# Optimization experiments

Measured on AMD Instinct MI355X. Metric: run time of the kernel, lower is better.

Reference implementation:

```python
import jax, jax.numpy as jnp
import numpy as np

N_NODES = 50000
N_EDGES = 800000
BASIS = 64
HIDDEN_RO = 128
N_GRAPHS = 512
T = 3


def setup_inputs() -> dict:
    key = jax.random.key(0)
    ks = jax.random.split(key, 12)
    Z = jax.random.randint(ks[0], (N_NODES,), 0, 10)
    edge_index = jax.random.randint(ks[1], (2, N_EDGES), 0, N_NODES)
    edge_attr = jax.random.normal(ks[2], (N_EDGES, BASIS), dtype=jnp.float32)
    batch = jnp.sort(jax.random.randint(ks[3], (N_NODES,), 0, N_GRAPHS))
    s = 1.0 / np.sqrt(BASIS)
    embed = jax.random.normal(ks[4], (10, BASIS), dtype=jnp.float32)
    cfW = jax.random.uniform(ks[5], (BASIS, BASIS), jnp.float32, -s, s)
    cfb = jax.random.uniform(ks[6], (BASIS,), jnp.float32, -s, s)
    dfW = jax.random.uniform(ks[7], (BASIS, BASIS), jnp.float32, -s, s)
    dfb = jax.random.uniform(ks[8], (BASIS,), jnp.float32, -s, s)
    fcW = jax.random.uniform(ks[9], (BASIS, BASIS), jnp.float32, -s, s)  # no bias
    W1 = jax.random.uniform(ks[10], (BASIS, HIDDEN_RO), jnp.float32, -s, s)
    b1 = jnp.zeros((HIDDEN_RO,), jnp.float32)
    W2 = jax.random.uniform(ks[11], (HIDDEN_RO, 4), jnp.float32, -1.0 / np.sqrt(HIDDEN_RO), 1.0 / np.sqrt(HIDDEN_RO))
    b2 = jnp.zeros((4,), jnp.float32)
    return {"Z": Z, "edge_index": edge_index, "edge_attr": edge_attr, "batch": batch,
            "embed": embed, "cfW": cfW, "cfb": cfb, "dfW": dfW, "dfb": dfb, "fcW": fcW,
            "W1": W1, "b1": b1, "W2": W2, "b2": b2}


def reference(Z, edge_index, edge_attr, batch, embed, cfW, cfb, dfW, dfb, fcW, W1, b1, W2, b2):
    src, dst = edge_index[0], edge_index[1]  # x_j gathered from src, aggregated at dst
    C = embed[Z]  # [N, basis]
    # df(edge_attr) does not depend on C; compute once (same math, shared weights)
    d_feat = edge_attr @ dfW + dfb  # [E, basis]
    for _ in range(T):
        c_feat = C[src] @ cfW + cfb            # gather + linear  [E, basis]
        msg = jnp.tanh((c_feat * d_feat) @ fcW)  # [E, basis]
        agg = jax.ops.segment_sum(msg, dst, num_segments=N_NODES)
        C = C + agg
    h = jnp.tanh(C @ W1 + b1) @ W2 + b2        # readout MLP [N, 4]
    return jax.ops.segment_sum(h, batch, num_segments=N_GRAPHS)  # global_add_pool [G, 4]
```

## Files before the change

kernel.cpp:

```cpp
#include <hip/hip_runtime.h>
#include <math.h>

#define N_NODES   50000
#define N_EDGES   800000
#define BASIS     64
#define HIDDEN_RO 128
#define N_GRAPHS  512
#define T_ITERS   3

typedef short s8 __attribute__((ext_vector_type(8)));
typedef float f4 __attribute__((ext_vector_type(4)));

#define MFMA16(a, b, c) __builtin_amdgcn_mfma_f32_16x16x32_bf16(a, b, c, 0, 0, 0)

__device__ __forceinline__ float fast_tanh(float x) {
    float e = __expf(2.0f * x);
    return 1.0f - 2.0f / (e + 1.0f);
}

__device__ __forceinline__ f4 splat4(float x) { f4 v; v[0]=x; v[1]=x; v[2]=x; v[3]=x; return v; }

__device__ __forceinline__ void split8(const float* x, s8& hi, s8& lo) {
    union { unsigned a[4]; s8 v; } H, L;
    #pragma unroll
    for (int j = 0; j < 4; ++j) {
        float e0 = x[2*j], e1 = x[2*j+1];
        unsigned u0 = __float_as_uint(e0), u1 = __float_as_uint(e1);
        H.a[j] = (u0 >> 16) | (u1 & 0xFFFF0000u);
        float l0 = e0 - __uint_as_float(u0 & 0xFFFF0000u);
        float l1 = e1 - __uint_as_float(u1 & 0xFFFF0000u);
        L.a[j] = (__float_as_uint(l0) >> 16) | (__float_as_uint(l1) & 0xFFFF0000u);
    }
    hi = H.v; lo = L.v;
}

__device__ __forceinline__ void load_wfrags(const float* __restrict__ W, int lane,
                                            s8 whi[2][4], s8 wlo[2][4]) {
    int q = lane >> 4, c = lane & 15;
    #pragma unroll
    for (int ks = 0; ks < 2; ++ks)
        #pragma unroll
        for (int g = 0; g < 4; ++g) {
            float t[8];
            #pragma unroll
            for (int j = 0; j < 8; ++j)
                t[j] = W[(ks*32 + q*8 + j) * 64 + g*16 + c];
            split8(t, whi[ks][g], wlo[ks][g]);
        }
}

__global__ void k_init_C(const int* __restrict__ Z, const float* __restrict__ embed,
                         float* __restrict__ C) {
    int i = blockIdx.x * blockDim.x + threadIdx.x;
    if (i >= N_NODES * BASIS) return;
    int n = i >> 6, c = i & 63;
    C[i] = embed[Z[n] * BASIS + c];
}

__global__ __launch_bounds__(256) void k_gemm64(const float* __restrict__ in,
        const float* __restrict__ W, const float* __restrict__ b,
        float* __restrict__ out, int rows) {
    int lane = threadIdx.x & 63, wv = threadIdx.x >> 6;
    int q = lane >> 4, c = lane & 15;
    s8 whi[2][4], wlo[2][4];
    load_wfrags(W, lane, whi, wlo);
    float bias[4];
    #pragma unroll
    for (int g = 0; g < 4; ++g) bias[g] = b[g*16 + c];
    int chunks = (rows + 15) >> 4;
    int wave = blockIdx.x * 4 + wv, nw = gridDim.x * 4;
    for (int ch = wave; ch < chunks; ch += nw) {
        int base = ch << 4;
        int row = base + c;
        bool valid = row < rows;
        const float4* ip = (const float4*)(in + (size_t)(valid ? row : 0) * 64);
        s8 ahi[2], alo[2];
        #pragma unroll
        for (int ks = 0; ks < 2; ++ks) {
            float4 a0 = ip[ks*8 + q*2 + 0];
            float4 a1 = ip[ks*8 + q*2 + 1];
            float xs[8] = {a0.x,a0.y,a0.z,a0.w, a1.x,a1.y,a1.z,a1.w};
            if (!valid) {
                #pragma unroll
                for (int j = 0; j < 8; ++j) xs[j] = 0.0f;
            }
            split8(xs, ahi[ks], alo[ks]);
        }
        f4 acc[4];
        #pragma unroll
        for (int g = 0; g < 4; ++g) acc[g] = splat4(bias[g]);
        #pragma unroll
        for (int ks = 0; ks < 2; ++ks)
            #pragma unroll
            for (int g = 0; g < 4; ++g) {
                acc[g] = MFMA16(ahi[ks], whi[ks][g], acc[g]);
                acc[g] = MFMA16(ahi[ks], wlo[ks][g], acc[g]);
                acc[g] = MFMA16(alo[ks], whi[ks][g], acc[g]);
            }
        #pragma unroll
        for (int g = 0; g < 4; ++g)
            #pragma unroll
            for (int r = 0; r < 4; ++r) {
                int ro = base + q*4 + r;
                if (ro < rows) out[(size_t)ro * 64 + g*16 + c] = acc[g][r];
            }
    }
}

__global__ void k_hist(const int* __restrict__ dst, int* __restrict__ deg) {
    int e = blockIdx.x * blockDim.x + threadIdx.x;
    if (e < N_EDGES) atomicAdd(&deg[dst[e]], 1);
}

__global__ void k_scan(const int* __restrict__ deg, int* __restrict__ off,
                       int* __restrict__ cursor) {
    __shared__ int wsum[16];
    __shared__ int run_s;
    int t = threadIdx.x, lane = t & 63, w = t >> 6;
    if (t == 0) run_s = 0;
    __syncthreads();
    for (int base = 0; base < N_NODES; base += 1024) {
        int i = base + t;
        int v = (i < N_NODES) ? deg[i] : 0;
        int s = v;
        #pragma unroll
        for (int ofs = 1; ofs < 64; ofs <<= 1) {
            int tmp = __shfl_up(s, ofs, 64);
            if (lane >= ofs) s += tmp;
        }
        if (lane == 63) wsum[w] = s;
        __syncthreads();
        if (w == 0) {
            int x = (lane < 16) ? wsum[lane] : 0;
            #pragma unroll
            for (int ofs = 1; ofs < 16; ofs <<= 1) {
                int tmp = __shfl_up(x, ofs, 64);
                if (lane >= ofs) x += tmp;
            }
            if (lane < 16) wsum[lane] = x;
        }
        __syncthreads();
        int run = run_s;
        int wex = (w == 0) ? 0 : wsum[w - 1];
        int incl = run + wex + s;
        if (i < N_NODES) { off[i] = incl - v; cursor[i] = incl - v; }
        __syncthreads();
        if (t == 1023) run_s = incl;
        __syncthreads();
    }
    if (t == 0) off[N_NODES] = run_s;
}

__global__ void k_fill(const int* __restrict__ dst, int* __restrict__ cursor,
                       int* __restrict__ eid) {
    int e = blockIdx.x * blockDim.x + threadIdx.x;
    if (e < N_EDGES) {
        int p = atomicAdd(&cursor[dst[e]], 1);
        eid[p] = e;
    }
}

__global__ __launch_bounds__(256) void k_mp_mfma(const float* __restrict__ CF,
        const float* __restrict__ DF, const float* __restrict__ fcW,
        const int* __restrict__ src, const int* __restrict__ off,
        const int* __restrict__ eid, float* __restrict__ C) {
    int lane = threadIdx.x & 63, wv = threadIdx.x >> 6;
    int q = lane >> 4, c = lane & 15;
    s8 whi[2][4], wlo[2][4];
    load_wfrags(fcW, lane, whi, wlo);
    int wave = blockIdx.x * 4 + wv, nw = gridDim.x * 4;
    for (int n = wave; n < N_NODES; n += nw) {
        int beg = off[n], end = off[n + 1];
        float acc0 = 0.f, acc1 = 0.f, acc2 = 0.f, acc3 = 0.f;
        #pragma unroll 1
        for (int base = beg; base < end; base += 16) {
            int cnt = end - base;
            bool valid = c < cnt;
            int idx = base + (valid ? c : 0);
            int e = eid[idx];
            int s = src[e];
            const float4* cfp = (const float4*)(CF + (size_t)s * 64);
            const float4* dfp = (const float4*)(DF + (size_t)e * 64);
            s8 ahi[2], alo[2];
            #pragma unroll
            for (int ks = 0; ks < 2; ++ks) {
                float4 c0 = cfp[ks*8 + q*2 + 0];
                float4 c1 = cfp[ks*8 + q*2 + 1];
                float4 d0 = dfp[ks*8 + q*2 + 0];
                float4 d1 = dfp[ks*8 + q*2 + 1];
                float xs[8] = {c0.x*d0.x, c0.y*d0.y, c0.z*d0.z, c0.w*d0.w,
                               c1.x*d1.x, c1.y*d1.y, c1.z*d1.z, c1.w*d1.w};
                if (!valid) {
                    #pragma unroll
                    for (int j = 0; j < 8; ++j) xs[j] = 0.0f;
                }
                split8(xs, ahi[ks], alo[ks]);
            }
            f4 d[4];
            #pragma unroll
            for (int g = 0; g < 4; ++g) d[g] = splat4(0.0f);
            #pragma unroll
            for (int ks = 0; ks < 2; ++ks)
                #pragma unroll
                for (int g = 0; g < 4; ++g) {
                    d[g] = MFMA16(ahi[ks], whi[ks][g], d[g]);
                    d[g] = MFMA16(ahi[ks], wlo[ks][g], d[g]);
                    d[g] = MFMA16(alo[ks], whi[ks][g], d[g]);
                }
            acc0 += fast_tanh(d[0][0]) + fast_tanh(d[0][1]) + fast_tanh(d[0][2]) + fast_tanh(d[0][3]);
            acc1 += fast_tanh(d[1][0]) + fast_tanh(d[1][1]) + fast_tanh(d[1][2]) + fast_tanh(d[1][3]);
            acc2 += fast_tanh(d[2][0]) + fast_tanh(d[2][1]) + fast_tanh(d[2][2]) + fast_tanh(d[2][3]);
            acc3 += fast_tanh(d[3][0]) + fast_tanh(d[3][1]) + fast_tanh(d[3][2]) + fast_tanh(d[3][3]);
        }
        acc0 += __shfl_xor(acc0, 16, 64); acc0 += __shfl_xor(acc0, 32, 64);
        acc1 += __shfl_xor(acc1, 16, 64); acc1 += __shfl_xor(acc1, 32, 64);
        acc2 += __shfl_xor(acc2, 16, 64); acc2 += __shfl_xor(acc2, 32, 64);
        acc3 += __shfl_xor(acc3, 16, 64); acc3 += __shfl_xor(acc3, 32, 64);
        float v = (q == 0) ? acc0 : (q == 1) ? acc1 : (q == 2) ? acc2 : acc3;
        C[(size_t)n * 64 + lane] += v;
    }
}

__global__ __launch_bounds__(256) void k_edge_fb(const float* __restrict__ CF,
        const float* __restrict__ ea, const float* __restrict__ dfW,
        const float* __restrict__ dfb, const float* __restrict__ fcW,
        const int* __restrict__ src, const int* __restrict__ dst,
        float* __restrict__ C) {
    int e = blockIdx.x * blockDim.x + threadIdx.x;
    if (e >= N_EDGES) return;
    int s = src[e], d = dst[e];
    float dfeat[BASIS];
    #pragma unroll
    for (int c = 0; c < BASIS; ++c) dfeat[c] = dfb[c];
    const float4* ea4 = (const float4*)(ea + (size_t)e * BASIS);
    #pragma unroll
    for (int k0 = 0; k0 < 16; ++k0) {
        float4 xv = ea4[k0];
        #pragma unroll
        for (int c = 0; c < BASIS; ++c)
            dfeat[c] += xv.x * dfW[(4*k0+0)*64+c] + xv.y * dfW[(4*k0+1)*64+c]
                      + xv.z * dfW[(4*k0+2)*64+c] + xv.w * dfW[(4*k0+3)*64+c];
    }
    const float4* cf4 = (const float4*)(CF + (size_t)s * BASIS);
    float acc[BASIS];
    #pragma unroll
    for (int c = 0; c < BASIS; ++c) acc[c] = 0.0f;
    #pragma unroll
    for (int k0 = 0; k0 < 16; ++k0) {
        float4 a = cf4[k0];
        float x0 = a.x * dfeat[4*k0+0], x1 = a.y * dfeat[4*k0+1];
        float x2 = a.z * dfeat[4*k0+2], x3 = a.w * dfeat[4*k0+3];
        #pragma unroll
        for (int c = 0; c < BASIS; ++c)
            acc[c] += x0 * fcW[(4*k0+0)*64+c] + x1 * fcW[(4*k0+1)*64+c]
                    + x2 * fcW[(4*k0+2)*64+c] + x3 * fcW[(4*k0+3)*64+c];
    }
    float* crow = C + (size_t)d * BASIS;
    #pragma unroll
    for (int c = 0; c < BASIS; ++c) atomicAdd(&crow[c], fast_tanh(acc[c]));
}

__global__ __launch_bounds__(256) void k_readout2(const float* __restrict__ C,
        const float* __restrict__ W1, const float* __restrict__ b1,
        const float* __restrict__ W2, const float* __restrict__ b2,
        const int* __restrict__ batch, float* __restrict__ out) {
    __shared__ float w1[BASIS * HIDDEN_RO];
    __shared__ float xbuf[4][64];
    int t = threadIdx.x;
    for (int i = t; i < BASIS * HIDDEN_RO; i += 256) w1[i] = W1[i];
    __syncthreads();
    int lane = t & 63, wv = t >> 6;
    float b1a = b1[lane], b1b = b1[64 + lane];
    float4 w2a = ((const float4*)W2)[lane];
    float4 w2b = ((const float4*)W2)[64 + lane];
    int wave = blockIdx.x * 4 + wv;
    int nw   = gridDim.x * 4;
    for (int n = wave; n < N_NODES; n += nw) {
        float x = C[(size_t)n * 64 + lane];
        xbuf[wv][lane] = x;
        __builtin_amdgcn_wave_barrier();
        const float4* xb = (const float4*)xbuf[wv];
        float sa = b1a, sb = b1b;
        #pragma unroll
        for (int k4 = 0; k4 < 16; ++k4) {
            float4 xv = xb[k4];
            const float* r0 = &w1[(4*k4 + 0) * HIDDEN_RO];
            const float* r1 = &w1[(4*k4 + 1) * HIDDEN_RO];
            const float* r2 = &w1[(4*k4 + 2) * HIDDEN_RO];
            const float* r3 = &w1[(4*k4 + 3) * HIDDEN_RO];
            sa += xv.x * r0[lane]      + xv.y * r1[lane]
                + xv.z * r2[lane]      + xv.w * r3[lane];
            sb += xv.x * r0[64 + lane] + xv.y * r1[64 + lane]
                + xv.z * r2[64 + lane] + xv.w * r3[64 + lane];
        }
        float ha = fast_tanh(sa), hb = fast_tanh(sb);
        float v0 = ha * w2a.x + hb * w2b.x;
        float v1 = ha * w2a.y + hb * w2b.y;
        float v2 = ha * w2a.z + hb * w2b.z;
        float v3 = ha * w2a.w + hb * w2b.w;
        #pragma unroll
        for (int ofs = 32; ofs >= 1; ofs >>= 1) {
            v0 += __shfl_down(v0, ofs, 64);
            v1 += __shfl_down(v1, ofs, 64);
            v2 += __shfl_down(v2, ofs, 64);
            v3 += __shfl_down(v3, ofs, 64);
        }
        if (lane == 0) {
            int g = batch[n];
            atomicAdd(&out[(size_t)g * 4 + 0], v0);
            atomicAdd(&out[(size_t)g * 4 + 1], v1);
            atomicAdd(&out[(size_t)g * 4 + 2], v2);
            atomicAdd(&out[(size_t)g * 4 + 3], v3);
        }
        __builtin_amdgcn_wave_barrier();
    }
}

extern "C" void kernel_launch(void* const* d_in, const int* in_sizes, int n_in,
                              void* d_out, int out_size, void* d_ws, size_t ws_size,
                              hipStream_t stream) {
    const int*   Z     = (const int*)d_in[0];
    const int*   ei    = (const int*)d_in[1];
    const float* ea    = (const float*)d_in[2];
    const int*   batch = (const int*)d_in[3];
    const float* embed = (const float*)d_in[4];
    const float* cfW   = (const float*)d_in[5];
    const float* cfb   = (const float*)d_in[6];
    const float* dfW   = (const float*)d_in[7];
    const float* dfb   = (const float*)d_in[8];
    const float* fcW   = (const float*)d_in[9];
    const float* W1    = (const float*)d_in[10];
    const float* b1    = (const float*)d_in[11];
    const float* W2    = (const float*)d_in[12];
    const float* b2    = (const float*)d_in[13];
    const int* src = ei;
    const int* dst = ei + N_EDGES;
    float* out = (float*)d_out;

    const size_t bC = (size_t)N_NODES * BASIS * sizeof(float);
    const size_t bE = (size_t)N_EDGES * sizeof(int);
    const size_t bO = (size_t)(N_NODES + 1) * sizeof(int);
    char* p = (char*)d_ws;
    float* C      = (float*)p;  p += bC;
    float* CF     = (float*)p;  p += bC;
    int*   eid    = (int*)p;    p += bE;
    int*   deg    = (int*)p;    p += bO;
    int*   off    = (int*)p;    p += bO;
    int*   cursor = (int*)p;    p += bO;
    float* DF     = (float*)p;
    const size_t need = (size_t)(p - (char*)d_ws) + (size_t)N_EDGES * BASIS * sizeof(float);
    const bool full = ws_size >= need;

    hipMemsetAsync(d_out, 0, (size_t)out_size * sizeof(float), stream);
    k_init_C<<<(N_NODES * BASIS + 255) / 256, 256, 0, stream>>>(Z, embed, C);

    if (full) {
        hipMemsetAsync(deg, 0, bO, stream);
        k_hist<<<(N_EDGES + 255) / 256, 256, 0, stream>>>(dst, deg);
        k_scan<<<1, 1024, 0, stream>>>(deg, off, cursor);
        k_fill<<<(N_EDGES + 255) / 256, 256, 0, stream>>>(dst, cursor, eid);
        k_gemm64<<<4096, 256, 0, stream>>>(ea, dfW, dfb, DF, N_EDGES);
        for (int t = 0; t < T_ITERS; ++t) {
            k_gemm64<<<800, 256, 0, stream>>>(C, cfW, cfb, CF, N_NODES);
            k_mp_mfma<<<2048, 256, 0, stream>>>(CF, DF, fcW, src, off, eid, C);
        }
    } else {
        for (int t = 0; t < T_ITERS; ++t) {
            k_gemm64<<<800, 256, 0, stream>>>(C, cfW, cfb, CF, N_NODES);
            k_edge_fb<<<(N_EDGES + 255) / 256, 256, 0, stream>>>(CF, ea, dfW, dfb, fcW, src, dst, C);
        }
    }

    k_readout2<<<512, 256, 0, stream>>>(C, W1, b1, W2, b2, batch, out);
}
```

Baseline: 979.4 us.

## Store DF in CSR order and process multi-node edge windows with LDS accumulation

The edge-feature GEMM now writes DF permuted into dst-sorted CSR order, using a packed int4 meta array (edge, src, dst). The message-passing kernel then reads DF contiguously instead of through an eid indirection. Each wave handles 4 consecutive nodes as one dense stream of 16-edge windows, which avoids padding waste on low-degree nodes. Results go into shared-memory accumulators through LDS atomics, and the next window's loads are software-prefetched. The costs are extra meta bandwidth, a gathered read of edge_attr, and LDS atomic contention.

```diff
diff --git a/kernel.cpp b/kernel.cpp
--- a/kernel.cpp
+++ b/kernel.cpp
@@ -7,6 +7,8 @@
 #define HIDDEN_RO 128
 #define N_GRAPHS  512
 #define T_ITERS   3
+#define R_NODES   4
+#define MP_BLOCKS (N_NODES / R_NODES / 4)
 
 typedef short s8 __attribute__((ext_vector_type(8)));
 typedef float f4 __attribute__((ext_vector_type(4)));
@@ -104,6 +106,49 @@
                 int ro = base + q*4 + r;
                 if (ro < rows) out[(size_t)ro * 64 + g*16 + c] = acc[g][r];
             }
+    }
+}
+
+__global__ __launch_bounds__(256) void k_gemm64g(const float* __restrict__ in,
+        const int4* __restrict__ meta, const float* __restrict__ W,
+        const float* __restrict__ b, float* __restrict__ out) {
+    int lane = threadIdx.x & 63, wv = threadIdx.x >> 6;
+    int q = lane >> 4, c = lane & 15;
+    s8 whi[2][4], wlo[2][4];
+    load_wfrags(W, lane, whi, wlo);
+    float bias[4];
+    #pragma unroll
+    for (int g = 0; g < 4; ++g) bias[g] = b[g*16 + c];
+    const int windows = N_EDGES / 16;
+    int wave = blockIdx.x * 4 + wv, nw = gridDim.x * 4;
+    for (int wb = wave; wb < windows; wb += nw) {
+        int slot = wb * 16 + c;
+        int e = meta[slot].x;
+        const float4* ip = (const float4*)(in + (size_t)e * 64);
+        s8 ahi[2], alo[2];
+        #pragma unroll
+        for (int ks = 0; ks < 2; ++ks) {
+            float4 a0 = ip[ks*8 + q*2 + 0];
+            float4 a1 = ip[ks*8 + q*2 + 1];
+            float xs[8] = {a0.x,a0.y,a0.z,a0.w, a1.x,a1.y,a1.z,a1.w};
+            split8(xs, ahi[ks], alo[ks]);
+        }
+        f4 acc[4];
+        #pragma unroll
+        for (int g = 0; g < 4; ++g) acc[g] = splat4(bias[g]);
+        #pragma unroll
+        for (int ks = 0; ks < 2; ++ks)
+            #pragma unroll
+            for (int g = 0; g < 4; ++g) {
+                acc[g] = MFMA16(ahi[ks], whi[ks][g], acc[g]);
+                acc[g] = MFMA16(ahi[ks], wlo[ks][g], acc[g]);
+                acc[g] = MFMA16(alo[ks], whi[ks][g], acc[g]);
+            }
+        #pragma unroll
+        for (int g = 0; g < 4; ++g)
+            #pragma unroll
+            for (int r = 0; r < 4; ++r)
+                out[(size_t)(wb*16 + q*4 + r) * 64 + g*16 + c] = acc[g][r];
     }
 }
 
@@ -151,73 +196,109 @@
     if (t == 0) off[N_NODES] = run_s;
 }
 
-__global__ void k_fill(const int* __restrict__ dst, int* __restrict__ cursor,
-                       int* __restrict__ eid) {
+__global__ void k_fill(const int* __restrict__ src, const int* __restrict__ dst,
+                       int* __restrict__ cursor, int4* __restrict__ meta) {
     int e = blockIdx.x * blockDim.x + threadIdx.x;
     if (e < N_EDGES) {
-        int p = atomicAdd(&cursor[dst[e]], 1);
-        eid[p] = e;
-    }
-}
-
-__global__ __launch_bounds__(256) void k_mp_mfma(const float* __restrict__ CF,
+        int d = dst[e], s = src[e];
+        int p = atomicAdd(&cursor[d], 1);
+        meta[p] = make_int4(e, s, d, 0);
+    }
+}
+
+__global__ __launch_bounds__(256) void k_mp_win(const float* __restrict__ CF,
         const float* __restrict__ DF, const float* __restrict__ fcW,
-        const int* __restrict__ src, const int* __restrict__ off,
-        const int* __restrict__ eid, float* __restrict__ C) {
+        const int4* __restrict__ meta, const int* __restrict__ off,
+        float* __restrict__ C) {
+    __shared__ float acc[4][R_NODES + 1][64];
     int lane = threadIdx.x & 63, wv = threadIdx.x >> 6;
     int q = lane >> 4, c = lane & 15;
     s8 whi[2][4], wlo[2][4];
     load_wfrags(fcW, lane, whi, wlo);
-    int wave = blockIdx.x * 4 + wv, nw = gridDim.x * 4;
-    for (int n = wave; n < N_NODES; n += nw) {
-        int beg = off[n], end = off[n + 1];
-        float acc0 = 0.f, acc1 = 0.f, acc2 = 0.f, acc3 = 0.f;
-        #pragma unroll 1
-        for (int base = beg; base < end; base += 16) {
-            int cnt = end - base;
-            bool valid = c < cnt;
-            int idx = base + (valid ? c : 0);
-            int e = eid[idx];
-            int s = src[e];
-            const float4* cfp = (const float4*)(CF + (size_t)s * 64);
-            const float4* dfp = (const float4*)(DF + (size_t)e * 64);
-            s8 ahi[2], alo[2];
-            #pragma unroll
-            for (int ks = 0; ks < 2; ++ks) {
-                float4 c0 = cfp[ks*8 + q*2 + 0];
-                float4 c1 = cfp[ks*8 + q*2 + 1];
-                float4 d0 = dfp[ks*8 + q*2 + 0];
-                float4 d1 = dfp[ks*8 + q*2 + 1];
-                float xs[8] = {c0.x*d0.x, c0.y*d0.y, c0.z*d0.z, c0.w*d0.w,
-                               c1.x*d1.x, c1.y*d1.y, c1.z*d1.z, c1.w*d1.w};
-                if (!valid) {
-                    #pragma unroll
-                    for (int j = 0; j < 8; ++j) xs[j] = 0.0f;
-                }
-                split8(xs, ahi[ks], alo[ks]);
-            }
-            f4 d[4];
-            #pragma unroll
-            for (int g = 0; g < 4; ++g) d[g] = splat4(0.0f);
-            #pragma unroll
-            for (int ks = 0; ks < 2; ++ks)
+    int wave = blockIdx.x * 4 + wv;
+    int n0 = wave * R_NODES;
+    int sbeg = off[n0], send = off[n0 + R_NODES];
+    #pragma unroll
+    for (int r = 0; r <= R_NODES; ++r) acc[wv][r][lane] = 0.0f;
+    __builtin_amdgcn_wave_barrier();
+    int nwin = (send - sbeg + 15) >> 4;
+
+    int4 m0 = make_int4(0,0,0,0), m1 = m0;
+    float4 dc[4], cf[4];
+    if (nwin > 0) {
+        int sl0 = sbeg + c; if (sl0 >= send) sl0 = send - 1;
+        m0 = meta[sl0];
+        if (nwin > 1) {
+            int sl1 = sbeg + 16 + c; if (sl1 >= send) sl1 = send - 1;
+            m1 = meta[sl1];
+        }
+        const float4* dp = (const float4*)(DF + (size_t)sl0 * 64);
+        dc[0] = dp[q*2]; dc[1] = dp[q*2+1]; dc[2] = dp[8+q*2]; dc[3] = dp[8+q*2+1];
+        const float4* cp = (const float4*)(CF + (size_t)m0.y * 64);
+        cf[0] = cp[q*2]; cf[1] = cp[q*2+1]; cf[2] = cp[8+q*2]; cf[3] = cp[8+q*2+1];
+    }
+    #pragma unroll 1
+    for (int w = 0; w < nwin; ++w) {
+        int base = sbeg + (w << 4);
+        bool valid = (base + c) < send;
+        int nloc = valid ? (m0.z - n0) : R_NODES;
+        float4 dn[4], cn[4];
+        int4 m2 = m1;
+        if (w + 1 < nwin) {
+            int sl = base + 16 + c; if (sl >= send) sl = send - 1;
+            const float4* dp = (const float4*)(DF + (size_t)sl * 64);
+            dn[0] = dp[q*2]; dn[1] = dp[q*2+1]; dn[2] = dp[8+q*2]; dn[3] = dp[8+q*2+1];
+            const float4* cp = (const float4*)(CF + (size_t)m1.y * 64);
+            cn[0] = cp[q*2]; cn[1] = cp[q*2+1]; cn[2] = cp[8+q*2]; cn[3] = cp[8+q*2+1];
+            if (w + 2 < nwin) {
+                int s2 = base + 32 + c; if (s2 >= send) s2 = send - 1;
+                m2 = meta[s2];
+            }
+        }
+        s8 ahi[2], alo[2];
+        {
+            float xs[8] = {cf[0].x*dc[0].x, cf[0].y*dc[0].y, cf[0].z*dc[0].z, cf[0].w*dc[0].w,
+                           cf[1].x*dc[1].x, cf[1].y*dc[1].y, cf[1].z*dc[1].z, cf[1].w*dc[1].w};
+            if (!valid) {
                 #pragma unroll
-                for (int g = 0; g < 4; ++g) {
-                    d[g] = MFMA16(ahi[ks], whi[ks][g], d[g]);
-                    d[g] = MFMA16(ahi[ks], wlo[ks][g], d[g]);
-                    d[g] = MFMA16(alo[ks], whi[ks][g], d[g]);
-                }
-            acc0 += fast_tanh(d[0][0]) + fast_tanh(d[0][1]) + fast_tanh(d[0][2]) + fast_tanh(d[0][3]);
-            acc1 += fast_tanh(d[1][0]) + fast_tanh(d[1][1]) + fast_tanh(d[1][2]) + fast_tanh(d[1][3]);
-            acc2 += fast_tanh(d[2][0]) + fast_tanh(d[2][1]) + fast_tanh(d[2][2]) + fast_tanh(d[2][3]);
-            acc3 += fast_tanh(d[3][0]) + fast_tanh(d[3][1]) + fast_tanh(d[3][2]) + fast_tanh(d[3][3]);
-        }
-        acc0 += __shfl_xor(acc0, 16, 64); acc0 += __shfl_xor(acc0, 32, 64);
-        acc1 += __shfl_xor(acc1, 16, 64); acc1 += __shfl_xor(acc1, 32, 64);
-        acc2 += __shfl_xor(acc2, 16, 64); acc2 += __shfl_xor(acc2, 32, 64);
-        acc3 += __shfl_xor(acc3, 16, 64); acc3 += __shfl_xor(acc3, 32, 64);
-        float v = (q == 0) ? acc0 : (q == 1) ? acc1 : (q == 2) ? acc2 : acc3;
-        C[(size_t)n * 64 + lane] += v;
+                for (int j = 0; j < 8; ++j) xs[j] = 0.0f;
+            }
+            split8(xs, ahi[0], alo[0]);
+            float ys[8] = {cf[2].x*dc[2].x, cf[2].y*dc[2].y, cf[2].z*dc[2].z, cf[2].w*dc[2].w,
+                           cf[3].x*dc[3].x, cf[3].y*dc[3].y, cf[3].z*dc[3].z, cf[3].w*dc[3].w};
+            if (!valid) {
+                #pragma unroll
+                for (int j = 0; j < 8; ++j) ys[j] = 0.0f;
+            }
+            split8(ys, ahi[1], alo[1]);
+        }
+        f4 d[4];
+        #pragma unroll
+        for (int g = 0; g < 4; ++g) d[g] = splat4(0.0f);
+        #pragma unroll
+        for (int ks = 0; ks < 2; ++ks)
+            #pragma unroll
+            for (int g = 0; g < 4; ++g) {
+                d[g] = MFMA16(ahi[ks], whi[ks][g], d[g]);
+                d[g] = MFMA16(ahi[ks], wlo[ks][g], d[g]);
+                d[g] = MFMA16(alo[ks], whi[ks][g], d[g]);
+            }
+        #pragma unroll
+        for (int r = 0; r < 4; ++r) {
+            int nl = __shfl(nloc, q*16 + q*4 + r, 64);
+            #pragma unroll
+            for (int g = 0; g < 4; ++g)
+                atomicAdd(&acc[wv][nl][g*16 + c], fast_tanh(d[g][r]));
+        }
+        m0 = m1; m1 = m2;
+        #pragma unroll
+        for (int i = 0; i < 4; ++i) { dc[i] = dn[i]; cf[i] = cn[i]; }
+    }
+    __syncthreads();
+    #pragma unroll
+    for (int r = 0; r < R_NODES; ++r) {
+        size_t ci = (size_t)(n0 + r) * 64 + lane;
+        C[ci] += acc[wv][r][lane];
     }
 }
 
@@ -338,12 +419,12 @@
     float* out = (float*)d_out;
 
     const size_t bC = (size_t)N_NODES * BASIS * sizeof(float);
-    const size_t bE = (size_t)N_EDGES * sizeof(int);
+    const size_t bM = (size_t)N_EDGES * sizeof(int4);
     const size_t bO = (size_t)(N_NODES + 1) * sizeof(int);
     char* p = (char*)d_ws;
     float* C      = (float*)p;  p += bC;
     float* CF     = (float*)p;  p += bC;
-    int*   eid    = (int*)p;    p += bE;
+    int4*  meta   = (int4*)p;   p += bM;
     int*   deg    = (int*)p;    p += bO;
     int*   off    = (int*)p;    p += bO;
     int*   cursor = (int*)p;    p += bO;
@@ -358,11 +439,11 @@
         hipMemsetAsync(deg, 0, bO, stream);
         k_hist<<<(N_EDGES + 255) / 256, 256, 0, stream>>>(dst, deg);
         k_scan<<<1, 1024, 0, stream>>>(deg, off, cursor);
-        k_fill<<<(N_EDGES + 255) / 256, 256, 0, stream>>>(dst, cursor, eid);
-        k_gemm64<<<4096, 256, 0, stream>>>(ea, dfW, dfb, DF, N_EDGES);
+        k_fill<<<(N_EDGES + 255) / 256, 256, 0, stream>>>(src, dst, cursor, meta);
+        k_gemm64g<<<4096, 256, 0, stream>>>(ea, meta, dfW, dfb, DF);
         for (int t = 0; t < T_ITERS; ++t) {
             k_gemm64<<<800, 256, 0, stream>>>(C, cfW, cfb, CF, N_NODES);
-            k_mp_mfma<<<2048, 256, 0, stream>>>(CF, DF, fcW, src, off, eid, C);
+            k_mp_win<<<MP_BLOCKS, 256, 0, stream>>>(CF, DF, fcW, meta, off, C);
         }
     } else {
         for (int t = 0; t < T_ITERS; ++t) {
```

Result: slower. 1.593 ms (+62.6%).

## Store DF in destination-sorted order and pre-pack weight fragments into LDS

Applied to the files above, without the earlier changes.

The edge-feature GEMM now gathers edge_attr rows through the CSR slot permutation, so DF is written in destination-sorted order. The message-passing kernel can then read DF contiguously per slot, and src ids sit in a parallel slot array, which removes the eid→src double indirection. Weights are split into bf16 hi/lo fragment images once by a small pack kernel and loaded into LDS per block instead of being rebuilt in registers. Init and histogram are fused into one kernel, the next chunk's src index is prefetched, and occupancy is hinted via launch bounds. In exchange, reading edge_attr becomes a scattered gather, and there is extra LDS traffic per MFMA.

```diff
diff --git a/kernel.cpp b/kernel.cpp
--- a/kernel.cpp
+++ b/kernel.cpp
@@ -34,82 +34,37 @@
     hi = H.v; lo = L.v;
 }
 
-__device__ __forceinline__ void load_wfrags(const float* __restrict__ W, int lane,
-                                            s8 whi[2][4], s8 wlo[2][4]) {
-    int q = lane >> 4, c = lane & 15;
-    #pragma unroll
-    for (int ks = 0; ks < 2; ++ks)
-        #pragma unroll
-        for (int g = 0; g < 4; ++g) {
-            float t[8];
-            #pragma unroll
-            for (int j = 0; j < 8; ++j)
-                t[j] = W[(ks*32 + q*8 + j) * 64 + g*16 + c];
-            split8(t, whi[ks][g], wlo[ks][g]);
-        }
-}
-
-__global__ void k_init_C(const int* __restrict__ Z, const float* __restrict__ embed,
-                         float* __restrict__ C) {
+__device__ __forceinline__ void packW_dev(const float* __restrict__ W, s8* __restrict__ img, int t) {
+    int lane = t & 63, q = lane >> 4, c = lane & 15;
+    int f0 = (t >> 6) * 2;
+    #pragma unroll
+    for (int f = f0; f < f0 + 2; ++f) {
+        int ks = f >> 2, g = f & 3;
+        float tv[8];
+        #pragma unroll
+        for (int j = 0; j < 8; ++j)
+            tv[j] = W[(ks*32 + q*8 + j) * 64 + g*16 + c];
+        s8 hi, lo;
+        split8(tv, hi, lo);
+        img[f * 64 + lane]       = hi;
+        img[(8 + f) * 64 + lane] = lo;
+    }
+}
+__global__ void k_packW(const float* __restrict__ W0, const float* __restrict__ W1,
+                        const float* __restrict__ W2, s8* __restrict__ i0,
+                        s8* __restrict__ i1, s8* __restrict__ i2) {
+    int b = blockIdx.x, t = threadIdx.x;
+    if (b == 0) packW_dev(W0, i0, t);
+    else if (b == 1) packW_dev(W1, i1, t);
+    else packW_dev(W2, i2, t);
+}
+
+__global__ void k_init_hist(const int* __restrict__ Z, const float* __restrict__ embed,
+                            float* __restrict__ C, const int* __restrict__ dst,
+                            int* __restrict__ deg) {
     int i = blockIdx.x * blockDim.x + threadIdx.x;
-    if (i >= N_NODES * BASIS) return;
-    int n = i >> 6, c = i & 63;
-    C[i] = embed[Z[n] * BASIS + c];
-}
-
-__global__ __launch_bounds__(256) void k_gemm64(const float* __restrict__ in,
-        const float* __restrict__ W, const float* __restrict__ b,
-        float* __restrict__ out, int rows) {
-    int lane = threadIdx.x & 63, wv = threadIdx.x >> 6;
-    int q = lane >> 4, c = lane & 15;
-    s8 whi[2][4], wlo[2][4];
-    load_wfrags(W, lane, whi, wlo);
-    float bias[4];
-    #pragma unroll
-    for (int g = 0; g < 4; ++g) bias[g] = b[g*16 + c];
-    int chunks = (rows + 15) >> 4;
-    int wave = blockIdx.x * 4 + wv, nw = gridDim.x * 4;
-    for (int ch = wave; ch < chunks; ch += nw) {
-        int base = ch << 4;
-        int row = base + c;
-        bool valid = row < rows;
-        const float4* ip = (const float4*)(in + (size_t)(valid ? row : 0) * 64);
-        s8 ahi[2], alo[2];
-        #pragma unroll
-        for (int ks = 0; ks < 2; ++ks) {
-            float4 a0 = ip[ks*8 + q*2 + 0];
-            float4 a1 = ip[ks*8 + q*2 + 1];
-            float xs[8] = {a0.x,a0.y,a0.z,a0.w, a1.x,a1.y,a1.z,a1.w};
-            if (!valid) {
-                #pragma unroll
-                for (int j = 0; j < 8; ++j) xs[j] = 0.0f;
-            }
-            split8(xs, ahi[ks], alo[ks]);
-        }
-        f4 acc[4];
-        #pragma unroll
-        for (int g = 0; g < 4; ++g) acc[g] = splat4(bias[g]);
-        #pragma unroll
-        for (int ks = 0; ks < 2; ++ks)
-            #pragma unroll
-            for (int g = 0; g < 4; ++g) {
-                acc[g] = MFMA16(ahi[ks], whi[ks][g], acc[g]);
-                acc[g] = MFMA16(ahi[ks], wlo[ks][g], acc[g]);
-                acc[g] = MFMA16(alo[ks], whi[ks][g], acc[g]);
-            }
-        #pragma unroll
-        for (int g = 0; g < 4; ++g)
-            #pragma unroll
-            for (int r = 0; r < 4; ++r) {
-                int ro = base + q*4 + r;
-                if (ro < rows) out[(size_t)ro * 64 + g*16 + c] = acc[g][r];
-            }
-    }
-}
-
-__global__ void k_hist(const int* __restrict__ dst, int* __restrict__ deg) {
-    int e = blockIdx.x * blockDim.x + threadIdx.x;
-    if (e < N_EDGES) atomicAdd(&deg[dst[e]], 1);
+    if (i < N_NODES * BASIS) { int n = i >> 6, c = i & 63; C[i] = embed[Z[n] * 64 + c]; }
+    if (i < N_EDGES) atomicAdd(&deg[dst[i]], 1);
 }
 
 __global__ void k_scan(const int* __restrict__ deg, int* __restrict__ off,
@@ -151,50 +106,122 @@
     if (t == 0) off[N_NODES] = run_s;
 }
 
-__global__ void k_fill(const int* __restrict__ dst, int* __restrict__ cursor,
-                       int* __restrict__ eid) {
+__global__ void k_fill(const int* __restrict__ src, const int* __restrict__ dst,
+                       int* __restrict__ cursor, int* __restrict__ slot_e,
+                       int* __restrict__ slot_s) {
     int e = blockIdx.x * blockDim.x + threadIdx.x;
     if (e < N_EDGES) {
-        int p = atomicAdd(&cursor[dst[e]], 1);
-        eid[p] = e;
-    }
-}
-
-__global__ __launch_bounds__(256) void k_mp_mfma(const float* __restrict__ CF,
-        const float* __restrict__ DF, const float* __restrict__ fcW,
-        const int* __restrict__ src, const int* __restrict__ off,
-        const int* __restrict__ eid, float* __restrict__ C) {
-    int lane = threadIdx.x & 63, wv = threadIdx.x >> 6;
-    int q = lane >> 4, c = lane & 15;
-    s8 whi[2][4], wlo[2][4];
-    load_wfrags(fcW, lane, whi, wlo);
+        int d = dst[e], s = src[e];
+        int p = atomicAdd(&cursor[d], 1);
+        slot_e[p] = e;
+        slot_s[p] = s;
+    }
+}
+
+template <int MODE>
+__global__ __launch_bounds__(256, 4) void k_gemm64L(const float* __restrict__ in,
+        const s8* __restrict__ wimg, const float* __restrict__ b,
+        const int* __restrict__ slot_e, float* __restrict__ out, int rows) {
+    __shared__ s8 LW[1024];
+    int t = threadIdx.x;
+    for (int i = t; i < 1024; i += 256) LW[i] = wimg[i];
+    __syncthreads();
+    int lane = t & 63, wv = t >> 6, q = lane >> 4, c = lane & 15;
+    float bias[4];
+    #pragma unroll
+    for (int g = 0; g < 4; ++g) bias[g] = b[g*16 + c];
+    int chunks = (rows + 15) >> 4;
+    int wave = blockIdx.x * 4 + wv, nw = gridDim.x * 4;
+    for (int ch = wave; ch < chunks; ch += nw) {
+        int base = ch << 4;
+        int row = base + c;
+        bool valid = row < rows;
+        int r = valid ? row : 0;
+        if (MODE == 1) r = slot_e[valid ? row : base];
+        const float4* ip = (const float4*)(in + (size_t)r * 64);
+        s8 ahi[2], alo[2];
+        #pragma unroll
+        for (int ks = 0; ks < 2; ++ks) {
+            float4 a0 = ip[ks*8 + q*2 + 0];
+            float4 a1 = ip[ks*8 + q*2 + 1];
+            float xs[8] = {a0.x,a0.y,a0.z,a0.w, a1.x,a1.y,a1.z,a1.w};
+            if (!valid) {
+                #pragma unroll
+                for (int j = 0; j < 8; ++j) xs[j] = 0.0f;
+            }
+            split8(xs, ahi[ks], alo[ks]);
+        }
+        f4 acc[4];
+        #pragma unroll
+        for (int g = 0; g < 4; ++g) acc[g] = splat4(bias[g]);
+        #pragma unroll
+        for (int ks = 0; ks < 2; ++ks)
+            #pragma unroll
+            for (int g = 0; g < 4; ++g) {
+                s8 wh = LW[(ks*4 + g) * 64 + lane];
+                s8 wl = LW[(8 + ks*4 + g) * 64 + lane];
+                acc[g] = MFMA16(ahi[ks], wh, acc[g]);
+                acc[g] = MFMA16(ahi[ks], wl, acc[g]);
+                acc[g] = MFMA16(alo[ks], wh, acc[g]);
+            }
+        #pragma unroll
+        for (int g = 0; g < 4; ++g)
+            #pragma unroll
+            for (int r2 = 0; r2 < 4; ++r2) {
+                int ro = base + q*4 + r2;
+                if (ro < rows) out[(size_t)ro * 64 + g*16 + c] = acc[g][r2];
+            }
+    }
+}
+
+__global__ __launch_bounds__(256, 4) void k_mp5(const float* __restrict__ CF,
+        const float* __restrict__ DF, const s8* __restrict__ wimg,
+        const int* __restrict__ slot_s, const int* __restrict__ off,
+        float* __restrict__ C) {
+    __shared__ s8 LW[1024];
+    int t = threadIdx.x;
+    for (int i = t; i < 1024; i += 256) LW[i] = wimg[i];
+    __syncthreads();
+    int lane = t & 63, wv = t >> 6, q = lane >> 4, c = lane & 15;
     int wave = blockIdx.x * 4 + wv, nw = gridDim.x * 4;
     for (int n = wave; n < N_NODES; n += nw) {
         int beg = off[n], end = off[n + 1];
+        if (beg >= end) continue;
         float acc0 = 0.f, acc1 = 0.f, acc2 = 0.f, acc3 = 0.f;
+        int sl0 = beg + c; if (sl0 >= end) sl0 = end - 1;
+        int srcn = slot_s[sl0];
         #pragma unroll 1
         for (int base = beg; base < end; base += 16) {
-            int cnt = end - base;
-            bool valid = c < cnt;
-            int idx = base + (valid ? c : 0);
-            int e = eid[idx];
-            int s = src[e];
-            const float4* cfp = (const float4*)(CF + (size_t)s * 64);
-            const float4* dfp = (const float4*)(DF + (size_t)e * 64);
+            int slot = base + c;
+            bool valid = slot < end;
+            if (!valid) slot = end - 1;
+            int scur = srcn;
+            if (base + 16 < end) {
+                int s2 = base + 16 + c; if (s2 >= end) s2 = end - 1;
+                srcn = slot_s[s2];
+            }
+            const float4* dp = (const float4*)(DF + (size_t)slot * 64);
+            float4 d0 = dp[q*2],     d1 = dp[q*2 + 1];
+            float4 d2 = dp[8 + q*2], d3 = dp[8 + q*2 + 1];
+            const float4* cp = (const float4*)(CF + (size_t)scur * 64);
+            float4 c0 = cp[q*2],     c1 = cp[q*2 + 1];
+            float4 c2 = cp[8 + q*2], c3 = cp[8 + q*2 + 1];
             s8 ahi[2], alo[2];
-            #pragma unroll
-            for (int ks = 0; ks < 2; ++ks) {
-                float4 c0 = cfp[ks*8 + q*2 + 0];
-                float4 c1 = cfp[ks*8 + q*2 + 1];
-                float4 d0 = dfp[ks*8 + q*2 + 0];
-                float4 d1 = dfp[ks*8 + q*2 + 1];
+            {
                 float xs[8] = {c0.x*d0.x, c0.y*d0.y, c0.z*d0.z, c0.w*d0.w,
                                c1.x*d1.x, c1.y*d1.y, c1.z*d1.z, c1.w*d1.w};
                 if (!valid) {
                     #pragma unroll
                     for (int j = 0; j < 8; ++j) xs[j] = 0.0f;
                 }
-                split8(xs, ahi[ks], alo[ks]);
+                split8(xs, ahi[0], alo[0]);
+                float ys[8] = {c2.x*d2.x, c2.y*d2.y, c2.z*d2.z, c2.w*d2.w,
+                               c3.x*d3.x, c3.y*d3.y, c3.z*d3.z, c3.w*d3.w};
+                if (!valid) {
+                    #pragma unroll
+                    for (int j = 0; j < 8; ++j) ys[j] = 0.0f;
+                }
+                split8(ys, ahi[1], alo[1]);
             }
             f4 d[4];
             #pragma unroll
@@ -203,9 +230,11 @@
             for (int ks = 0; ks < 2; ++ks)
                 #pragma unroll
                 for (int g = 0; g < 4; ++g) {
-                    d[g] = MFMA16(ahi[ks], whi[ks][g], d[g]);
-                    d[g] = MFMA16(ahi[ks], wlo[ks][g], d[g]);
-                    d[g] = MFMA16(alo[ks], whi[ks][g], d[g]);
+                    s8 wh = LW[(ks*4 + g) * 64 + lane];
+                    s8 wl = LW[(8 + ks*4 + g) * 64 + lane];
+                    d[g] = MFMA16(ahi[ks], wh, d[g]);
+                    d[g] = MFMA16(ahi[ks], wl, d[g]);
+                    d[g] = MFMA16(alo[ks], wh, d[g]);
                 }
             acc0 += fast_tanh(d[0][0]) + fast_tanh(d[0][1]) + fast_tanh(d[0][2]) + fast_tanh(d[0][3]);
             acc1 += fast_tanh(d[1][0]) + fast_tanh(d[1][1]) + fast_tanh(d[1][2]) + fast_tanh(d[1][3]);
@@ -221,6 +250,26 @@
     }
 }
 
+__global__ __launch_bounds__(256) void k_gemm64_fb(const float* __restrict__ in,
+        const float* __restrict__ W, const float* __restrict__ b,
+        float* __restrict__ out, int rows) {
+    int r = blockIdx.x * blockDim.x + threadIdx.x;
+    if (r >= rows) return;
+    float acc[BASIS];
+    #pragma unroll
+    for (int c = 0; c < BASIS; ++c) acc[c] = b[c];
+    const float4* in4 = (const float4*)(in + (size_t)r * BASIS);
+    #pragma unroll 1
+    for (int k0 = 0; k0 < 16; ++k0) {
+        float4 xv = in4[k0];
+        #pragma unroll
+        for (int c = 0; c < BASIS; ++c)
+            acc[c] += xv.x * W[(4*k0+0)*64+c] + xv.y * W[(4*k0+1)*64+c]
+                    + xv.z * W[(4*k0+2)*64+c] + xv.w * W[(4*k0+3)*64+c];
+    }
+    #pragma unroll
+    for (int c = 0; c < BASIS; ++c) out[(size_t)r * BASIS + c] = acc[c];
+}
 __global__ __launch_bounds__(256) void k_edge_fb(const float* __restrict__ CF,
         const float* __restrict__ ea, const float* __restrict__ dfW,
         const float* __restrict__ dfb, const float* __restrict__ fcW,
@@ -340,33 +389,40 @@
     const size_t bC = (size_t)N_NODES * BASIS * sizeof(float);
     const size_t bE = (size_t)N_EDGES * sizeof(int);
     const size_t bO = (size_t)(N_NODES + 1) * sizeof(int);
+    const size_t bI = 1024 * sizeof(s8);
     char* p = (char*)d_ws;
     float* C      = (float*)p;  p += bC;
     float* CF     = (float*)p;  p += bC;
-    int*   eid    = (int*)p;    p += bE;
+    int*   slotE  = (int*)p;    p += bE;
+    int*   slotS  = (int*)p;    p += bE;
     int*   deg    = (int*)p;    p += bO;
     int*   off    = (int*)p;    p += bO;
     int*   cursor = (int*)p;    p += bO;
-    float* DF     = (float*)p;
+    p = (char*)(((uintptr_t)p + 255) & ~(uintptr_t)255);
+    s8* imgDF = (s8*)p;  p += bI;
+    s8* imgCF = (s8*)p;  p += bI;
+    s8* imgFC = (s8*)p;  p += bI;
+    float* DF = (float*)p;
     const size_t need = (size_t)(p - (char*)d_ws) + (size_t)N_EDGES * BASIS * sizeof(float);
     const bool full = ws_size >= need;
 
     hipMemsetAsync(d_out, 0, (size_t)out_size * sizeof(float), stream);
-    k_init_C<<<(N_NODES * BASIS + 255) / 256, 256, 0, stream>>>(Z, embed, C);
 
     if (full) {
         hipMemsetAsync(deg, 0, bO, stream);
-        k_hist<<<(N_EDGES + 255) / 256, 256, 0, stream>>>(dst, deg);
+        k_init_hist<<<(N_NODES * BASIS + 255) / 256, 256, 0, stream>>>(Z, embed, C, dst, deg);
+        k_packW<<<3, 256, 0, stream>>>(dfW, cfW, fcW, imgDF, imgCF, imgFC);
         k_scan<<<1, 1024, 0, stream>>>(deg, off, cursor);
-        k_fill<<<(N_EDGES + 255) / 256, 256, 0, stream>>>(dst, cursor, eid);
-        k_gemm64<<<4096, 256, 0, stream>>>(ea, dfW, dfb, DF, N_EDGES);
+        k_fill<<<(N_EDGES + 255) / 256, 256, 0, stream>>>(src, dst, cursor, slotE, slotS);
+        k_gemm64L<1><<<4096, 256, 0, stream>>>(ea, imgDF, dfb, slotE, DF, N_EDGES);
         for (int t = 0; t < T_ITERS; ++t) {
-            k_gemm64<<<800, 256, 0, stream>>>(C, cfW, cfb, CF, N_NODES);
-            k_mp_mfma<<<2048, 256, 0, stream>>>(CF, DF, fcW, src, off, eid, C);
+            k_gemm64L<0><<<800, 256, 0, stream>>>(C, imgCF, cfb, nullptr, CF, N_NODES);
+            k_mp5<<<2048, 256, 0, stream>>>(CF, DF, imgFC, slotS, off, C);
         }
     } else {
+        k_init_hist<<<(N_NODES * BASIS + 255) / 256, 256, 0, stream>>>(Z, embed, C, dst, (int*)CF);
         for (int t = 0; t < T_ITERS; ++t) {
-            k_gemm64<<<800, 256, 0, stream>>>(C, cfW, cfb, CF, N_NODES);
+            k_gemm64_fb<<<(N_NODES + 255) / 256, 256, 0, stream>>>(C, cfW, cfb, CF, N_NODES);
             k_edge_fb<<<(N_EDGES + 255) / 256, 256, 0, stream>>>(CF, ea, dfW, dfb, fcW, src, dst, C);
         }
     }
```

Result: faster. 926.2 us (-5.4%).
